# Kernel optimization log

Measured on AMD Instinct MI355X. Metric: run time of the kernel, lower is better.

The kernel has to match this reference:

```python
import jax, jax.numpy as jnp
import numpy as np
from jax import lax

B, C, H, W = 8, 64, 128, 128
K = 3           # kernel size
KK = K * K
PAD = K // 2
EPS = 1e-5


def setup_inputs() -> dict:
    key = jax.random.key(0)
    ks = jax.random.split(key, 12)
    s = lambda fan: 1.0 / np.sqrt(fan)
    return {
        "x":      jax.random.normal(ks[0], (B, C, H, W), jnp.float32),
        # offset-predicting conv of the deformable conv: 2*KK offset channels
        "off_w":  jax.random.normal(ks[1], (2 * KK, C, K, K), jnp.float32) * (0.01 * s(C * KK)),
        "off_b":  jnp.zeros((2 * KK,), jnp.float32),
        # deformable conv main weight
        "dw":     jax.random.normal(ks[2], (C, C, K, K), jnp.float32) * s(C * KK),
        "db":     jax.random.normal(ks[3], (C,), jnp.float32) * 0.01,
        # weight_conv1 (1x1)
        "w1":     jax.random.normal(ks[4], (C, C), jnp.float32) * s(C),
        "b1":     jax.random.normal(ks[5], (C,), jnp.float32) * 0.01,
        # BatchNorm (eval mode: running stats)
        "gamma":  jnp.ones((C,), jnp.float32),
        "beta":   jnp.zeros((C,), jnp.float32),
        "rmean":  jax.random.normal(ks[6], (C,), jnp.float32) * 0.01,
        "rvar":   jax.random.uniform(ks[7], (C,), jnp.float32, 0.5, 1.5),
        # weight_conv2 (1x1, downsample=False)
        "w2":     jax.random.normal(ks[8], (C, C), jnp.float32) * s(C),
        "b2":     jax.random.normal(ks[9], (C,), jnp.float32) * 0.01,
    }


def _avg_pool3(x):
    # AvgPool2d(3, stride=1, padding=1), count_include_pad=True (torch default)
    s = lax.reduce_window(x, 0.0, lax.add, (1, 1, 3, 3), (1, 1, 1, 1),
                          [(0, 0), (0, 0), (1, 1), (1, 1)])
    return s / 9.0


def _deform_conv(p, off_w, off_b, dw, db):
    # offsets: [B, 2*KK, H, W] -> [B, KK, 2(y,x), H, W]
    off = lax.conv_general_dilated(p, off_w, (1, 1), [(PAD, PAD), (PAD, PAD)],
                                   dimension_numbers=("NCHW", "OIHW", "NCHW"))
    off = off + off_b[None, :, None, None]
    off = off.reshape(B, KK, 2, H, W)

    # base sampling grid: p0 + pk
    hh = jnp.arange(H, dtype=p.dtype)[:, None]          # [H,1]
    ww = jnp.arange(W, dtype=p.dtype)[None, :]          # [1,W]
    ky = (jnp.arange(KK) // K - PAD).astype(p.dtype)    # [KK]
    kx = (jnp.arange(KK) % K - PAD).astype(p.dtype)
    sy = hh[None, None] + ky[None, :, None, None] + off[:, :, 0]   # [B,KK,H,W]
    sx = ww[None, None] + kx[None, :, None, None] + off[:, :, 1]

    y0 = jnp.floor(sy); x0 = jnp.floor(sx)
    wy = sy - y0;        wx = sx - x0
    y0 = y0.astype(jnp.int32); x0 = x0.astype(jnp.int32)

    pf = p.reshape(B, C, H * W)

    def corner(yc, xc, w):
        valid = ((yc >= 0) & (yc < H) & (xc >= 0) & (xc < W))
        idx = jnp.clip(yc, 0, H - 1) * W + jnp.clip(xc, 0, W - 1)   # [B,KK,H,W]
        g = jax.vmap(lambda f, i: f[:, i])(pf, idx)                  # [B,C,KK,H,W]
        return g * (w * valid.astype(p.dtype))[:, None]

    sampled = (corner(y0,     x0,     (1 - wy) * (1 - wx)) +
               corner(y0,     x0 + 1, (1 - wy) * wx) +
               corner(y0 + 1, x0,     wy * (1 - wx)) +
               corner(y0 + 1, x0 + 1, wy * wx))                      # [B,C,KK,H,W]

    out = jnp.einsum("bckhw,ock->bohw", sampled, dw.reshape(C, C, KK))
    return out + db[None, :, None, None]


def reference(x, off_w, off_b, dw, db, w1, b1, gamma, beta, rmean, rvar, w2, b2):
    p = _avg_pool3(x)
    r = _deform_conv(p, off_w, off_b, dw, db)
    # weight_conv1 (1x1) + BN (eval) + ReLU
    h = jnp.einsum("bchw,oc->bohw", r, w1) + b1[None, :, None, None]
    inv = gamma / jnp.sqrt(rvar + EPS)
    h = h * inv[None, :, None, None] + (beta - rmean * inv)[None, :, None, None]
    h = jax.nn.relu(h)
    h = x + h
    # weight_conv2 (1x1, downsample=False)
    return jnp.einsum("bchw,oc->bohw", h, w2) + b2[None, :, None, None]
```

## Files before the change

kernel.cpp:

```cpp
#include <hip/hip_runtime.h>
#include <hip/hip_bf16.h>
#include <cstddef>

#define H_ 128
#define W_ 128
#define HW_ 16384
#define C_ 64
#define B_ 8
#define EPS_ 1e-5f

#define KSLOTS 18
#define ROWS 584
#define TSTR 64
#define OTSTR 64

typedef __attribute__((ext_vector_type(8))) short bf16x8;
typedef __attribute__((ext_vector_type(4))) float f32x4;
typedef __attribute__((ext_vector_type(2))) float f32x2;

__device__ __forceinline__ unsigned short f2bf(float f) {
  __hip_bfloat16 h = __float2bfloat16(f);
  unsigned short u;
  __builtin_memcpy(&u, &h, 2);
  return u;
}
__device__ __forceinline__ unsigned pack2(float lo, float hi) {
  return (unsigned)f2bf(lo) | ((unsigned)f2bf(hi) << 16);
}
__device__ __forceinline__ float bfl(unsigned short v) {
  return __uint_as_float(((unsigned)v) << 16);
}

__global__ __launch_bounds__(256) void pool_prep_kernel(
    const float* __restrict__ xin, unsigned short* __restrict__ pbf,
    const float* __restrict__ dw, const float* __restrict__ offw,
    const float* __restrict__ w1, const float* __restrict__ b1,
    const float* __restrict__ gamma, const float* __restrict__ beta,
    const float* __restrict__ rmean, const float* __restrict__ rvar,
    const float* __restrict__ w2,
    unsigned short* __restrict__ wf2, unsigned short* __restrict__ offwp,
    unsigned short* __restrict__ w1p, unsigned short* __restrict__ w2p,
    float* __restrict__ b1f) {
  int t = threadIdx.x;
  int blk = blockIdx.x;
  if (blk >= 2048) {
    int i = (blk - 2048) * 256 + t;
    if (i < 36864) {
      int j = i & 7, l = (i >> 3) & 63, og = (i >> 9) & 3, sg = i >> 11;
      int o = og * 16 + (l & 15);
      int k = sg * 32 + ((l >> 4) << 3) + j;
      int kk = k >> 6, c = k & 63;
      wf2[i] = f2bf(dw[o * 576 + c * 9 + kk]);
    } else if (i < 36864 + 18432) {
      int j2 = i - 36864;
      int j = j2 & 7, l = (j2 >> 3) & 63, og = (j2 >> 9) & 1, slot = j2 >> 10;
      int kk = slot >> 1, s = slot & 1;
      int oc = og * 16 + (l & 15);
      int c = s * 32 + ((l >> 4) << 3) + j;
      float v = (oc < 18) ? offw[oc * 576 + c * 9 + kk] : 0.f;
      offwp[j2] = f2bf(v);
    } else if (i < 36864 + 18432 + 4096) {
      int j2 = i - 36864 - 18432;
      int j = j2 & 7, l = (j2 >> 3) & 63, og = (j2 >> 9) & 3, sg = j2 >> 11;
      int o = og * 16 + (l & 15);
      int c = sg * 32 + ((l >> 4) << 3) + j;
      float inv = gamma[o] * rsqrtf(rvar[o] + EPS_);
      w1p[j2] = f2bf(w1[o * 64 + c] * inv);
    } else if (i < 36864 + 18432 + 8192) {
      int j2 = i - 36864 - 18432 - 4096;
      int j = j2 & 7, l = (j2 >> 3) & 63, og = (j2 >> 9) & 3, sg = j2 >> 11;
      int o = og * 16 + (l & 15);
      int c = sg * 32 + ((l >> 4) << 3) + j;
      w2p[j2] = f2bf(w2[o * 64 + c]);
    } else if (i < 36864 + 18432 + 8192 + 64) {
      int o = i - 36864 - 18432 - 8192;
      float inv = gamma[o] * rsqrtf(rvar[o] + EPS_);
      b1f[o] = b1[o] * inv + beta[o] - rmean[o] * inv;
    }
    return;
  }
  __shared__ __align__(16) unsigned short pool[64 * 72];
  int c = t & 63, wvp = t >> 6;
  int half = blk & 1;
  int row = blk >> 1;
  int b = row >> 7, y = row & 127;
  int xb = half * 64 + wvp * 16;
  const float* q = xin + (size_t)(b * C_ + c) * HW_;

  float ver[16];
#pragma unroll
  for (int i = 0; i < 16; ++i) ver[i] = 0.f;
#pragma unroll
  for (int dy = -1; dy <= 1; ++dy) {
    int yy = y + dy;
    if ((unsigned)yy < 128u) {
      const float* r = q + yy * W_;
      float m[18];
      m[0] = (xb > 0) ? r[xb - 1] : 0.f;
      float4 v0 = *(const float4*)(r + xb);
      float4 v1 = *(const float4*)(r + xb + 4);
      float4 v2 = *(const float4*)(r + xb + 8);
      float4 v3 = *(const float4*)(r + xb + 12);
      m[1] = v0.x; m[2] = v0.y; m[3] = v0.z; m[4] = v0.w;
      m[5] = v1.x; m[6] = v1.y; m[7] = v1.z; m[8] = v1.w;
      m[9] = v2.x; m[10] = v2.y; m[11] = v2.z; m[12] = v2.w;
      m[13] = v3.x; m[14] = v3.y; m[15] = v3.z; m[16] = v3.w;
      m[17] = (xb < 112) ? r[xb + 16] : 0.f;
#pragma unroll
      for (int i = 0; i < 16; ++i) ver[i] += m[i] + m[i + 1] + m[i + 2];
    }
  }
  int pxb = wvp * 16;
#pragma unroll
  for (int i = 0; i < 16; ++i) {
    int px = pxb + i;
    int cg = c >> 3;
    pool[px * 72 + ((cg ^ (px & 7)) << 3) + (c & 7)] = f2bf(ver[i] * (1.f / 9.f));
  }
  __syncthreads();

  size_t base = ((size_t)(b * HW_) + y * W_ + half * 64) * 64;
#pragma unroll
  for (int k = 0; k < 2; ++k) {
    int ch = k * 256 + t;
    int px = ch >> 3, g = ch & 7;
    uint2 v = *(const uint2*)(pool + px * 72 + ((g ^ (px & 7)) << 3));
    uint2 v2 = *(const uint2*)(pool + px * 72 + ((g ^ (px & 7)) << 3) + 4);
    *(uint4*)(pbf + base + px * 64 + g * 8) = make_uint4(v.x, v.y, v2.x, v2.y);
  }
}

__global__ __launch_bounds__(256, 4) void offconv_kernel(
    const unsigned short* __restrict__ pbf, const unsigned short* __restrict__ offwp,
    const float* __restrict__ offb, unsigned short* __restrict__ offo) {
  __shared__ __align__(16) unsigned short tile[198 * OTSTR];
  __shared__ unsigned short offTb[18 * 64];
  int t = threadIdx.x;
  int lane = t & 63, wv = t >> 6;
  int l15 = lane & 15, lp = lane >> 4;
  int blk = blockIdx.x;
  int half = blk & 1;
  int row = blk >> 1;
  int b = row >> 7, y = row & 127;
  int x0 = half * 64;

#pragma unroll
  for (int it = 0; it < 7; ++it) {
    int ch = it * 256 + t;
    if (ch < 1584) {
      int rc = ch >> 3, g = ch & 7;
      int r = rc / 66, cx = rc - r * 66;
      int iy = y - 1 + r, ix = x0 - 1 + cx;
      uint4 v = make_uint4(0u, 0u, 0u, 0u);
      if (((unsigned)iy < 128u) && ((unsigned)ix < 128u)) {
        v = *(const uint4*)(pbf + ((size_t)(b * HW_) + iy * W_ + ix) * 64 + g * 8);
      }
      *(uint4*)(tile + rc * OTSTR + ((g ^ (rc & 7)) << 3)) = v;
    }
  }
  __syncthreads();

  int og = wv & 1;
  int oc = og * 16 + l15;
  float bo = offb[min(oc, 17)];
  const bf16x8* ofp = (const bf16x8*)offwp;
#pragma unroll
  for (int pti = 0; pti < 2; ++pti) {
    int pt = (wv >> 1) + pti * 2;
    f32x4 aco = (f32x4){bo, bo, bo, bo};
#pragma unroll
    for (int kk = 0; kk < 9; ++kk) {
      int rowb = (kk / 3) * 66 + (kk % 3) + pt * 16 + l15;
#pragma unroll
      for (int s = 0; s < 2; ++s) {
        int ga = s * 4 + lp;
        bf16x8 a = *(const bf16x8*)(tile + rowb * OTSTR + ((ga ^ (rowb & 7)) << 3));
        bf16x8 bw = ofp[((kk * 2 + s) * 2 + og) * 64 + lane];
        aco = __builtin_amdgcn_mfma_f32_16x16x32_bf16(a, bw, aco, 0, 0, 0);
      }
    }
    if (oc < 18) {
#pragma unroll
      for (int j = 0; j < 4; ++j) offTb[oc * 64 + pt * 16 + lp * 4 + j] = f2bf(aco[j]);
    }
  }
  __syncthreads();

#pragma unroll
  for (int it = 0; it < 3; ++it) {
    int idx = it * 256 + t;
    if (idx < 576) {
      int oc2 = idx >> 5, pxp = (idx & 31) * 2;
      unsigned v = (unsigned)offTb[oc2 * 64 + pxp] |
                   ((unsigned)offTb[oc2 * 64 + pxp + 1] << 16);
      *(unsigned*)(offo + (size_t)(b * 18 + oc2) * HW_ + y * W_ + x0 + pxp) = v;
    }
  }
}

__global__ __launch_bounds__(256, 4) void deform_kernel(
    const unsigned short* __restrict__ pbf, const unsigned short* __restrict__ offo,
    const unsigned short* __restrict__ wf2, const unsigned short* __restrict__ w1p,
    const unsigned short* __restrict__ w2p, const float* __restrict__ db,
    const float* __restrict__ b1f, const float* __restrict__ b2,
    const float* __restrict__ xin, float* __restrict__ out) {
  __shared__ __align__(16) unsigned short tileTb[100 * TSTR];
  __shared__ __align__(16) unsigned short sAb[16 * ROWS];
  __shared__ __align__(16) unsigned short rTb[16 * 72];
  __shared__ __align__(16) unsigned short hTb[16 * 72];
  __shared__ uint2 cwb[144];
  __shared__ uchar4 rel4[144];
  __shared__ int wOK[4];
  int t = threadIdx.x;
  int lane = t & 63, wv = t >> 6;
  int l15 = lane & 15, lp = lane >> 4;
  int pix0 = blockIdx.x * 16;
  int b = pix0 >> 14;
  int yx0 = pix0 & 16383;
  int y = yx0 >> 7, x0 = yx0 & 127;
  int ty = min(max(y - 2, 0), 123);
  int tx = min(max(x0 - 2, 0), 108);
  const unsigned short* pB = pbf + (size_t)(b * HW_) * 64;

  int o_me = wv * 16 + l15;
  int px0 = lp * 4;
  const float4 xv = *(const float4*)(xin + (size_t)(b * C_ + o_me) * HW_ + yx0 + px0);

  const bf16x8* wfp = (const bf16x8*)wf2;
  bf16x8 bwr0 = wfp[(0 * 4 + wv) * 64 + lane];
  bf16x8 bwr1 = wfp[(1 * 4 + wv) * 64 + lane];
  bf16x8 bwr2 = wfp[(2 * 4 + wv) * 64 + lane];
  bf16x8 bwr3 = wfp[(3 * 4 + wv) * 64 + lane];
  bf16x8 bwr4 = wfp[(4 * 4 + wv) * 64 + lane];
  bf16x8 bwr5 = wfp[(5 * 4 + wv) * 64 + lane];
  bf16x8 bwr6 = wfp[(6 * 4 + wv) * 64 + lane];
  bf16x8 bwr7 = wfp[(7 * 4 + wv) * 64 + lane];
  bf16x8 bwr8 = wfp[(8 * 4 + wv) * 64 + lane];

  bool ok = true;
  int pixl = t & 15, kk = t >> 4;
  bool active = (t < 144);
  if (active) {
    int xx = x0 + pixl;
    const unsigned short* ob = offo + (size_t)(b * 18 + kk * 2) * HW_ + y * W_ + xx;
    float offy = bfl(ob[0]);
    float offx = bfl(ob[HW_]);
    float sy = (float)(y + (kk / 3) - 1) + offy;
    float sx = (float)(xx + (kk % 3) - 1) + offx;
    float fy = floorf(sy), fx = floorf(sx);
    float wy = sy - fy, wx = sx - fx;
    int iy = (int)fy, ix = (int)fx;
    float w[4];
    int rc[4];
#pragma unroll
    for (int j = 0; j < 4; ++j) {
      int dy = j >> 1, dx = j & 1;
      int yc = iy + dy, xc = ix + dx;
      bool v = ((unsigned)yc < 128u) && ((unsigned)xc < 128u);
      int ycc = min(max(yc, 0), 127), xcc = min(max(xc, 0), 127);
      float wgt = (dy ? wy : 1.f - wy) * (dx ? wx : 1.f - wx);
      w[j] = v ? wgt : 0.f;
      bool in_tile = (ycc >= ty) && (ycc <= ty + 4) && (xcc >= tx) && (xcc <= tx + 19);
      ok = ok && ((w[j] == 0.f) || in_tile);
      int ry = min(max(ycc - ty, 0), 4);
      int rx = min(max(xcc - tx, 0), 19);
      rc[j] = ry * 20 + rx;
    }
    cwb[t] = make_uint2(pack2(w[0], w[1]), pack2(w[2], w[3]));
    rel4[t] = make_uchar4((unsigned char)rc[0], (unsigned char)rc[1],
                          (unsigned char)rc[2], (unsigned char)rc[3]);
  }
  {
    unsigned long long m = __ballot(ok);
    if (lane == 0) wOK[wv] = (m == ~0ull) ? 1 : 0;
  }

#pragma unroll
  for (int it = 0; it < 3; ++it) {
    int ch = it * 256 + t;
    int rc = ch >> 3, g = ch & 7;
    int r = rc / 20, cx = rc - r * 20;
    uint4 v = *(const uint4*)(pB + ((size_t)((ty + r) * W_ + tx + cx)) * 64 + g * 8);
    *(uint4*)(tileTb + rc * TSTR + ((g ^ (rc & 7)) << 3)) = v;
  }
  if (t < 32) {
    int ch = 768 + t;
    int rc = ch >> 3, g = ch & 7;
    int r = rc / 20, cx = rc - r * 20;
    uint4 v = *(const uint4*)(pB + ((size_t)((ty + r) * W_ + tx + cx)) * 64 + g * 8);
    *(uint4*)(tileTb + rc * TSTR + ((g ^ (rc & 7)) << 3)) = v;
  }
  __syncthreads();

  bool fast = wOK[0] && wOK[1] && wOK[2] && wOK[3];

  if (fast) {
    auto do_gran = [&](int n) {
      int job = n >> 3, g = n & 7;
      int jp = job & 15, jk = job >> 4;
      uint2 wp = cwb[job];
      uchar4 rl = rel4[job];
      float w0 = bfl((unsigned short)(wp.x & 0xffffu));
      float w1_ = bfl((unsigned short)(wp.x >> 16));
      float w2_ = bfl((unsigned short)(wp.y & 0xffffu));
      float w3_ = bfl((unsigned short)(wp.y >> 16));
      bf16x8 v0 = *(const bf16x8*)(tileTb + (int)rl.x * TSTR + ((g ^ (rl.x & 7)) << 3));
      bf16x8 v1 = *(const bf16x8*)(tileTb + (int)rl.y * TSTR + ((g ^ (rl.y & 7)) << 3));
      bf16x8 v2 = *(const bf16x8*)(tileTb + (int)rl.z * TSTR + ((g ^ (rl.z & 7)) << 3));
      bf16x8 v3 = *(const bf16x8*)(tileTb + (int)rl.w * TSTR + ((g ^ (rl.w & 7)) << 3));
      const unsigned* u0 = (const unsigned*)&v0;
      const unsigned* u1 = (const unsigned*)&v1;
      const unsigned* u2 = (const unsigned*)&v2;
      const unsigned* u3 = (const unsigned*)&v3;
      unsigned dws[4];
#pragma unroll
      for (int d = 0; d < 4; ++d) {
        f32x2 c0 = {__uint_as_float(u0[d] << 16), __uint_as_float(u0[d] & 0xffff0000u)};
        f32x2 c1 = {__uint_as_float(u1[d] << 16), __uint_as_float(u1[d] & 0xffff0000u)};
        f32x2 c2 = {__uint_as_float(u2[d] << 16), __uint_as_float(u2[d] & 0xffff0000u)};
        f32x2 c3 = {__uint_as_float(u3[d] << 16), __uint_as_float(u3[d] & 0xffff0000u)};
        f32x2 s = w0 * c0 + w1_ * c1 + w2_ * c2 + w3_ * c3;
        dws[d] = pack2(s[0], s[1]);
      }
      *(uint4*)(sAb + jp * ROWS + jk * 64 + g * 8) =
          make_uint4(dws[0], dws[1], dws[2], dws[3]);
    };
    do_gran(t);
    do_gran(t + 256);
    do_gran(t + 512);
    do_gran(t + 768);
    if (t < 128) do_gran(t + 1024);
  } else {
    if (active) {
      int xx = x0 + pixl;
      const unsigned short* ob = offo + (size_t)(b * 18 + kk * 2) * HW_ + y * W_ + xx;
      float offy = bfl(ob[0]);
      float offx = bfl(ob[HW_]);
      float sy = (float)(y + (kk / 3) - 1) + offy;
      float sx = (float)(xx + (kk % 3) - 1) + offx;
      float fy = floorf(sy), fx = floorf(sx);
      float wy = sy - fy, wx = sx - fx;
      int iy = (int)fy, ix = (int)fx;
      float wj[4];
      const unsigned short* pc[4];
#pragma unroll
      for (int j = 0; j < 4; ++j) {
        int dy = j >> 1, dx = j & 1;
        int yc = iy + dy, xc = ix + dx;
        bool v = ((unsigned)yc < 128u) && ((unsigned)xc < 128u);
        int ycc = min(max(yc, 0), 127), xcc = min(max(xc, 0), 127);
        wj[j] = v ? (dy ? wy : 1.f - wy) * (dx ? wx : 1.f - wx) : 0.f;
        pc[j] = pB + ((size_t)(ycc * W_ + xcc)) * 64;
      }
      unsigned short* wr = sAb + pixl * ROWS + kk * 64;
#pragma unroll 4
      for (int c = 0; c < 64; ++c) {
        float v = wj[0] * bfl(pc[0][c]) + wj[1] * bfl(pc[1][c]) +
                  wj[2] * bfl(pc[2][c]) + wj[3] * bfl(pc[3][c]);
        wr[c] = f2bf(v);
      }
    }
  }
  __syncthreads();

  f32x4 acc;
  {
    float d = db[o_me];
    acc = (f32x4){d, d, d, d};
  }
  const unsigned short* arow = sAb + l15 * ROWS + (lp << 3);
#define MF(s, bwv)                                                           \
  {                                                                          \
    bf16x8 a = *(const bf16x8*)(arow + (s) * 32);                            \
    acc = __builtin_amdgcn_mfma_f32_16x16x32_bf16(a, (bwv), acc, 0, 0, 0);   \
  }
  MF(0, bwr0) MF(1, bwr1) MF(2, bwr2) MF(3, bwr3) MF(4, bwr4)
  MF(5, bwr5) MF(6, bwr6) MF(7, bwr7) MF(8, bwr8)
#pragma unroll
  for (int s = 9; s < KSLOTS; ++s) {
    bf16x8 a = *(const bf16x8*)(arow + s * 32);
    bf16x8 bw = wfp[(s * 4 + wv) * 64 + lane];
    acc = __builtin_amdgcn_mfma_f32_16x16x32_bf16(a, bw, acc, 0, 0, 0);
  }
#undef MF

#pragma unroll
  for (int j = 0; j < 4; ++j) {
    rTb[(px0 + j) * 72 + o_me] = f2bf(acc[j]);
  }
  __syncthreads();

  f32x4 acc1;
  {
    float bb = b1f[o_me];
    acc1 = (f32x4){bb, bb, bb, bb};
  }
  const unsigned short* arow1 = rTb + l15 * 72 + (lp << 3);
  const bf16x8* w1f8 = (const bf16x8*)w1p;
#pragma unroll
  for (int s = 0; s < 2; ++s) {
    bf16x8 a = *(const bf16x8*)(arow1 + s * 32);
    bf16x8 bw = w1f8[(s * 4 + wv) * 64 + lane];
    acc1 = __builtin_amdgcn_mfma_f32_16x16x32_bf16(a, bw, acc1, 0, 0, 0);
  }
  float h0 = fmaxf(acc1[0], 0.f) + xv.x;
  float h1 = fmaxf(acc1[1], 0.f) + xv.y;
  float h2 = fmaxf(acc1[2], 0.f) + xv.z;
  float h3 = fmaxf(acc1[3], 0.f) + xv.w;
  hTb[(px0 + 0) * 72 + o_me] = f2bf(h0);
  hTb[(px0 + 1) * 72 + o_me] = f2bf(h1);
  hTb[(px0 + 2) * 72 + o_me] = f2bf(h2);
  hTb[(px0 + 3) * 72 + o_me] = f2bf(h3);
  __syncthreads();

  f32x4 acc2;
  {
    float bo = b2[o_me];
    acc2 = (f32x4){bo, bo, bo, bo};
  }
  const unsigned short* arow2 = hTb + l15 * 72 + (lp << 3);
  const bf16x8* w2f8 = (const bf16x8*)w2p;
#pragma unroll
  for (int s = 0; s < 2; ++s) {
    bf16x8 a = *(const bf16x8*)(arow2 + s * 32);
    bf16x8 bw = w2f8[(s * 4 + wv) * 64 + lane];
    acc2 = __builtin_amdgcn_mfma_f32_16x16x32_bf16(a, bw, acc2, 0, 0, 0);
  }
  *(float4*)(out + (size_t)(b * C_ + o_me) * HW_ + yx0 + px0) =
      make_float4(acc2[0], acc2[1], acc2[2], acc2[3]);
}

extern "C" void kernel_launch(void* const* d_in, const int* in_sizes, int n_in,
                              void* d_out, int out_size, void* d_ws, size_t ws_size,
                              hipStream_t stream) {
  const float* x = (const float*)d_in[0];
  const float* offw = (const float*)d_in[1];
  const float* offb = (const float*)d_in[2];
  const float* dw = (const float*)d_in[3];
  const float* db = (const float*)d_in[4];
  const float* w1 = (const float*)d_in[5];
  const float* b1 = (const float*)d_in[6];
  const float* gamma = (const float*)d_in[7];
  const float* beta = (const float*)d_in[8];
  const float* rmean = (const float*)d_in[9];
  const float* rvar = (const float*)d_in[10];
  const float* w2 = (const float*)d_in[11];
  const float* b2 = (const float*)d_in[12];
  float* out = (float*)d_out;

  unsigned short* pbf = (unsigned short*)d_ws;
  unsigned short* offo = pbf + 8388608;
  unsigned short* wf2 = offo + 2359296;
  unsigned short* offwp = wf2 + 36864;
  unsigned short* w1p = offwp + 18432;
  unsigned short* w2p = w1p + 4096;
  float* b1f = (float*)(w2p + 4096);

  pool_prep_kernel<<<2305, 256, 0, stream>>>(x, pbf, dw, offw, w1, b1, gamma,
                                             beta, rmean, rvar, w2, wf2, offwp,
                                             w1p, w2p, b1f);
  offconv_kernel<<<2048, 256, 0, stream>>>(pbf, offwp, offb, offo);
  deform_kernel<<<8192, 256, 0, stream>>>(pbf, offo, wf2, w1p, w2p, db, b1f, b2,
                                          x, out);
}
```

Measured before the change: 102.1 us.

## Process 32 pixels per block with 512 threads to share the sampling tile

The deform kernel now handles 32 pixels per block with 8 waves, split into 4 output-channel groups and 2 pixel halves. The staged input tile grows to 5x36 positions, so halo overhead per pixel shrinks and the tile load is amortised over twice as many pixels. The first nine deformable-conv weight fragments are no longer preloaded into registers before the sampling phase; all weights are now fetched inside the MFMA loop. The launch bound changes to 512 threads with 2 blocks per CU, and the larger LDS footprint per block may reduce occupancy. The wider tile may also push more blocks onto the slow path when offsets fall outside it.

```diff
diff --git a/kernel.cpp b/kernel.cpp
--- a/kernel.cpp
+++ b/kernel.cpp
@@ -13,6 +13,7 @@
 #define ROWS 584
 #define TSTR 64
 #define OTSTR 64
+#define TROWS 180
 
 typedef __attribute__((ext_vector_type(8))) short bf16x8;
 typedef __attribute__((ext_vector_type(4))) float f32x4;
@@ -198,48 +199,38 @@
   }
 }
 
-__global__ __launch_bounds__(256, 4) void deform_kernel(
+__global__ __launch_bounds__(512, 2) void deform_kernel(
     const unsigned short* __restrict__ pbf, const unsigned short* __restrict__ offo,
     const unsigned short* __restrict__ wf2, const unsigned short* __restrict__ w1p,
     const unsigned short* __restrict__ w2p, const float* __restrict__ db,
     const float* __restrict__ b1f, const float* __restrict__ b2,
     const float* __restrict__ xin, float* __restrict__ out) {
-  __shared__ __align__(16) unsigned short tileTb[100 * TSTR];
-  __shared__ __align__(16) unsigned short sAb[16 * ROWS];
-  __shared__ __align__(16) unsigned short rTb[16 * 72];
-  __shared__ __align__(16) unsigned short hTb[16 * 72];
-  __shared__ uint2 cwb[144];
-  __shared__ uchar4 rel4[144];
-  __shared__ int wOK[4];
+  __shared__ __align__(16) unsigned short tileTb[TROWS * TSTR];
+  __shared__ __align__(16) unsigned short sAb[32 * ROWS];
+  __shared__ __align__(16) unsigned short rTb[32 * 72];
+  __shared__ __align__(16) unsigned short hTb[32 * 72];
+  __shared__ uint2 cwb[288];
+  __shared__ uchar4 rel4[288];
+  __shared__ int wOK[8];
   int t = threadIdx.x;
   int lane = t & 63, wv = t >> 6;
   int l15 = lane & 15, lp = lane >> 4;
-  int pix0 = blockIdx.x * 16;
+  int og = wv & 3, ph = wv >> 2;
+  int pix0 = blockIdx.x * 32;
   int b = pix0 >> 14;
   int yx0 = pix0 & 16383;
   int y = yx0 >> 7, x0 = yx0 & 127;
   int ty = min(max(y - 2, 0), 123);
-  int tx = min(max(x0 - 2, 0), 108);
+  int tx = min(max(x0 - 2, 0), 92);
   const unsigned short* pB = pbf + (size_t)(b * HW_) * 64;
 
-  int o_me = wv * 16 + l15;
-  int px0 = lp * 4;
-  const float4 xv = *(const float4*)(xin + (size_t)(b * C_ + o_me) * HW_ + yx0 + px0);
-
-  const bf16x8* wfp = (const bf16x8*)wf2;
-  bf16x8 bwr0 = wfp[(0 * 4 + wv) * 64 + lane];
-  bf16x8 bwr1 = wfp[(1 * 4 + wv) * 64 + lane];
-  bf16x8 bwr2 = wfp[(2 * 4 + wv) * 64 + lane];
-  bf16x8 bwr3 = wfp[(3 * 4 + wv) * 64 + lane];
-  bf16x8 bwr4 = wfp[(4 * 4 + wv) * 64 + lane];
-  bf16x8 bwr5 = wfp[(5 * 4 + wv) * 64 + lane];
-  bf16x8 bwr6 = wfp[(6 * 4 + wv) * 64 + lane];
-  bf16x8 bwr7 = wfp[(7 * 4 + wv) * 64 + lane];
-  bf16x8 bwr8 = wfp[(8 * 4 + wv) * 64 + lane];
+  int o_me = og * 16 + l15;
+  int px0q = ph * 16 + lp * 4;
+  const float4 xv = *(const float4*)(xin + (size_t)(b * C_ + o_me) * HW_ + yx0 + px0q);
 
   bool ok = true;
-  int pixl = t & 15, kk = t >> 4;
-  bool active = (t < 144);
+  int pixl = t & 31, kk = t >> 5;
+  bool active = (t < 288);
   if (active) {
     int xx = x0 + pixl;
     const unsigned short* ob = offo + (size_t)(b * 18 + kk * 2) * HW_ + y * W_ + xx;
@@ -260,11 +251,11 @@
       int ycc = min(max(yc, 0), 127), xcc = min(max(xc, 0), 127);
       float wgt = (dy ? wy : 1.f - wy) * (dx ? wx : 1.f - wx);
       w[j] = v ? wgt : 0.f;
-      bool in_tile = (ycc >= ty) && (ycc <= ty + 4) && (xcc >= tx) && (xcc <= tx + 19);
+      bool in_tile = (ycc >= ty) && (ycc <= ty + 4) && (xcc >= tx) && (xcc <= tx + 35);
       ok = ok && ((w[j] == 0.f) || in_tile);
       int ry = min(max(ycc - ty, 0), 4);
-      int rx = min(max(xcc - tx, 0), 19);
-      rc[j] = ry * 20 + rx;
+      int rx = min(max(xcc - tx, 0), 35);
+      rc[j] = ry * 36 + rx;
     }
     cwb[t] = make_uint2(pack2(w[0], w[1]), pack2(w[2], w[3]));
     rel4[t] = make_uchar4((unsigned char)rc[0], (unsigned char)rc[1],
@@ -276,28 +267,29 @@
   }
 
 #pragma unroll
-  for (int it = 0; it < 3; ++it) {
-    int ch = it * 256 + t;
+  for (int it = 0; it < 2; ++it) {
+    int ch = it * 512 + t;
     int rc = ch >> 3, g = ch & 7;
-    int r = rc / 20, cx = rc - r * 20;
+    int r = rc / 36, cx = rc - r * 36;
     uint4 v = *(const uint4*)(pB + ((size_t)((ty + r) * W_ + tx + cx)) * 64 + g * 8);
     *(uint4*)(tileTb + rc * TSTR + ((g ^ (rc & 7)) << 3)) = v;
   }
-  if (t < 32) {
-    int ch = 768 + t;
+  if (t < 416) {
+    int ch = 1024 + t;
     int rc = ch >> 3, g = ch & 7;
-    int r = rc / 20, cx = rc - r * 20;
+    int r = rc / 36, cx = rc - r * 36;
     uint4 v = *(const uint4*)(pB + ((size_t)((ty + r) * W_ + tx + cx)) * 64 + g * 8);
     *(uint4*)(tileTb + rc * TSTR + ((g ^ (rc & 7)) << 3)) = v;
   }
   __syncthreads();
 
-  bool fast = wOK[0] && wOK[1] && wOK[2] && wOK[3];
+  bool fast = wOK[0] && wOK[1] && wOK[2] && wOK[3] &&
+              wOK[4] && wOK[5] && wOK[6] && wOK[7];
 
   if (fast) {
     auto do_gran = [&](int n) {
       int job = n >> 3, g = n & 7;
-      int jp = job & 15, jk = job >> 4;
+      int jp = job & 31, jk = job >> 5;
       uint2 wp = cwb[job];
       uchar4 rl = rel4[job];
       float w0 = bfl((unsigned short)(wp.x & 0xffffu));
@@ -326,10 +318,10 @@
           make_uint4(dws[0], dws[1], dws[2], dws[3]);
     };
     do_gran(t);
-    do_gran(t + 256);
     do_gran(t + 512);
-    do_gran(t + 768);
-    if (t < 128) do_gran(t + 1024);
+    do_gran(t + 1024);
+    do_gran(t + 1536);
+    if (t < 256) do_gran(t + 2048);
   } else {
     if (active) {
       int xx = x0 + pixl;
@@ -368,25 +360,18 @@
     float d = db[o_me];
     acc = (f32x4){d, d, d, d};
   }
-  const unsigned short* arow = sAb + l15 * ROWS + (lp << 3);
-#define MF(s, bwv)                                                           \
-  {                                                                          \
-    bf16x8 a = *(const bf16x8*)(arow + (s) * 32);                            \
-    acc = __builtin_amdgcn_mfma_f32_16x16x32_bf16(a, (bwv), acc, 0, 0, 0);   \
-  }
-  MF(0, bwr0) MF(1, bwr1) MF(2, bwr2) MF(3, bwr3) MF(4, bwr4)
-  MF(5, bwr5) MF(6, bwr6) MF(7, bwr7) MF(8, bwr8)
-#pragma unroll
-  for (int s = 9; s < KSLOTS; ++s) {
+  const unsigned short* arow = sAb + (ph * 16 + l15) * ROWS + (lp << 3);
+  const bf16x8* wfp = (const bf16x8*)wf2;
+#pragma unroll
+  for (int s = 0; s < KSLOTS; ++s) {
     bf16x8 a = *(const bf16x8*)(arow + s * 32);
-    bf16x8 bw = wfp[(s * 4 + wv) * 64 + lane];
+    bf16x8 bw = wfp[(s * 4 + og) * 64 + lane];
     acc = __builtin_amdgcn_mfma_f32_16x16x32_bf16(a, bw, acc, 0, 0, 0);
   }
-#undef MF
 
 #pragma unroll
   for (int j = 0; j < 4; ++j) {
-    rTb[(px0 + j) * 72 + o_me] = f2bf(acc[j]);
+    rTb[(px0q + j) * 72 + o_me] = f2bf(acc[j]);
   }
   __syncthreads();
 
@@ -395,22 +380,22 @@
     float bb = b1f[o_me];
     acc1 = (f32x4){bb, bb, bb, bb};
   }
-  const unsigned short* arow1 = rTb + l15 * 72 + (lp << 3);
+  const unsigned short* arow1 = rTb + (ph * 16 + l15) * 72 + (lp << 3);
   const bf16x8* w1f8 = (const bf16x8*)w1p;
 #pragma unroll
   for (int s = 0; s < 2; ++s) {
     bf16x8 a = *(const bf16x8*)(arow1 + s * 32);
-    bf16x8 bw = w1f8[(s * 4 + wv) * 64 + lane];
+    bf16x8 bw = w1f8[(s * 4 + og) * 64 + lane];
     acc1 = __builtin_amdgcn_mfma_f32_16x16x32_bf16(a, bw, acc1, 0, 0, 0);
   }
   float h0 = fmaxf(acc1[0], 0.f) + xv.x;
   float h1 = fmaxf(acc1[1], 0.f) + xv.y;
   float h2 = fmaxf(acc1[2], 0.f) + xv.z;
   float h3 = fmaxf(acc1[3], 0.f) + xv.w;
-  hTb[(px0 + 0) * 72 + o_me] = f2bf(h0);
-  hTb[(px0 + 1) * 72 + o_me] = f2bf(h1);
-  hTb[(px0 + 2) * 72 + o_me] = f2bf(h2);
-  hTb[(px0 + 3) * 72 + o_me] = f2bf(h3);
+  hTb[(px0q + 0) * 72 + o_me] = f2bf(h0);
+  hTb[(px0q + 1) * 72 + o_me] = f2bf(h1);
+  hTb[(px0q + 2) * 72 + o_me] = f2bf(h2);
+  hTb[(px0q + 3) * 72 + o_me] = f2bf(h3);
   __syncthreads();
 
   f32x4 acc2;
@@ -418,15 +403,15 @@
     float bo = b2[o_me];
     acc2 = (f32x4){bo, bo, bo, bo};
   }
-  const unsigned short* arow2 = hTb + l15 * 72 + (lp << 3);
+  const unsigned short* arow2 = hTb + (ph * 16 + l15) * 72 + (lp << 3);
   const bf16x8* w2f8 = (const bf16x8*)w2p;
 #pragma unroll
   for (int s = 0; s < 2; ++s) {
     bf16x8 a = *(const bf16x8*)(arow2 + s * 32);
-    bf16x8 bw = w2f8[(s * 4 + wv) * 64 + lane];
+    bf16x8 bw = w2f8[(s * 4 + og) * 64 + lane];
     acc2 = __builtin_amdgcn_mfma_f32_16x16x32_bf16(a, bw, acc2, 0, 0, 0);
   }
-  *(float4*)(out + (size_t)(b * C_ + o_me) * HW_ + yx0 + px0) =
+  *(float4*)(out + (size_t)(b * C_ + o_me) * HW_ + yx0 + px0q) =
       make_float4(acc2[0], acc2[1], acc2[2], acc2[3]);
 }
 
@@ -460,6 +445,6 @@
                                              beta, rmean, rvar, w2, wf2, offwp,
                                              w1p, w2p, b1f);
   offconv_kernel<<<2048, 256, 0, stream>>>(pbf, offwp, offb, offo);
-  deform_kernel<<<8192, 256, 0, stream>>>(pbf, offo, wf2, w1p, w2p, db, b1f, b2,
+  deform_kernel<<<4096, 512, 0, stream>>>(pbf, offo, wf2, w1p, w2p, db, b1f, b2,
                                           x, out);
 }
```

Measured after the change: 110.8 us. 1.09x slower.
